# Optimization experiments

Measured on AMD Instinct MI355X. Metric: run time of the kernel, lower is better.

Reference implementation:

```python
import jax, jax.numpy as jnp
import numpy as np

N = 100000   # nodes
E = 1600000  # edges (avg degree 16)
G = 512      # graphs in batch
IN = 96      # in_channels
H = 128      # hidden_channels
C = 100      # num_classes
ED = 8       # edge_dim
L = 4        # num_layers
EPS_LN = 1e-5


def setup_inputs() -> dict:
    key = jax.random.key(0)
    ks = jax.random.split(key, 24)
    s = 0.05
    d = {
        "x": jax.random.normal(ks[0], (N, IN), jnp.float32),
        "edge_index": jax.random.randint(ks[1], (2, E), 0, N, jnp.int32),
        "batch": jnp.sort(jax.random.randint(ks[2], (N,), 0, G, jnp.int32)),
        "edge_attr": jax.random.normal(ks[3], (E, ED), jnp.float32),
        # edge encoder MLP: Linear(ED,H) -> ReLU -> Linear(H,1)
        "ee_W1": jax.random.normal(ks[4], (ED, H), jnp.float32) * s,
        "ee_b1": jnp.zeros((H,), jnp.float32),
        "ee_W2": jax.random.normal(ks[5], (H, 1), jnp.float32) * s,
        "ee_b2": jnp.zeros((1,), jnp.float32),
        # GCNConv weights (PyG: lin without bias, bias added after aggregation)
        "W0": jax.random.normal(ks[6], (IN, H), jnp.float32) * s,
        "cb0": jnp.zeros((H,), jnp.float32),
        "W1": jax.random.normal(ks[7], (H, H), jnp.float32) * s,
        "cb1": jnp.zeros((H,), jnp.float32),
        "W2": jax.random.normal(ks[8], (H, H), jnp.float32) * s,
        "cb2": jnp.zeros((H,), jnp.float32),
        "W3": jax.random.normal(ks[9], (H, H), jnp.float32) * s,
        "cb3": jnp.zeros((H,), jnp.float32),
        # LayerNorm params
        "g0": jnp.ones((H,), jnp.float32), "be0": jnp.zeros((H,), jnp.float32),
        "g1": jnp.ones((H,), jnp.float32), "be1": jnp.zeros((H,), jnp.float32),
        "g2": jnp.ones((H,), jnp.float32), "be2": jnp.zeros((H,), jnp.float32),
        "g3": jnp.ones((H,), jnp.float32), "be3": jnp.zeros((H,), jnp.float32),
        # residual projection for layer 0 only (IN != H)
        "res_W": jax.random.normal(ks[10], (IN, H), jnp.float32) * s,
        "res_b": jnp.zeros((H,), jnp.float32),
        # head: Linear(2H,H) -> ReLU -> Linear(H,C)
        "hW1": jax.random.normal(ks[11], (2 * H, H), jnp.float32) * s,
        "hb1": jnp.zeros((H,), jnp.float32),
        "hW2": jax.random.normal(ks[12], (H, C), jnp.float32) * s,
        "hb2": jnp.zeros((C,), jnp.float32),
    }
    return d


def _layer_norm(h, g, b):
    mu = jnp.mean(h, axis=-1, keepdims=True)
    var = jnp.mean(jnp.square(h - mu), axis=-1, keepdims=True)
    return g * (h - mu) / jnp.sqrt(var + EPS_LN) + b


def reference(x, edge_index, batch, edge_attr,
              ee_W1, ee_b1, ee_W2, ee_b2,
              W0, cb0, W1, cb1, W2, cb2, W3, cb3,
              g0, be0, g1, be1, g2, be2, g3, be3,
              res_W, res_b, hW1, hb1, hW2, hb2):
    row, col = edge_index[0], edge_index[1]

    # edge weight = softplus(MLP(edge_attr)) + 1e-4  -> [E]
    eh = jax.nn.relu(edge_attr @ ee_W1 + ee_b1)
    ew = jax.nn.softplus((eh @ ee_W2 + ee_b2)[:, 0]) + 1e-4

    # add self loops with weight 1 (PyG GCNConv default)
    loops = jnp.arange(N, dtype=row.dtype)
    row_sl = jnp.concatenate([row, loops])
    col_sl = jnp.concatenate([col, loops])
    ew_sl = jnp.concatenate([ew, jnp.ones((N,), ew.dtype)])

    # symmetric normalization: D^-1/2 A D^-1/2 (deg over target index)
    deg = jax.ops.segment_sum(ew_sl, col_sl, num_segments=N)
    dis = jnp.where(deg > 0, jax.lax.rsqrt(deg), 0.0)
    norm = dis[row_sl] * ew_sl * dis[col_sl]  # [E+N]

    def conv(h, W, b):
        hw = h @ W                                   # [N,H]
        msg = hw[row_sl] * norm[:, None]             # [E+N,H]
        return jax.ops.segment_sum(msg, col_sl, num_segments=N) + b

    Ws = [W0, W1, W2, W3]
    cbs = [cb0, cb1, cb2, cb3]
    gs = [g0, g1, g2, g3]
    bes = [be0, be1, be2, be3]

    hidden = []
    cur = x
    for i in range(L):
        h = conv(cur, Ws[i], cbs[i])
        h = _layer_norm(h, gs[i], bes[i])
        res = cur @ res_W + res_b if i == 0 else cur
        h = jax.nn.relu(h + res)
        # dropout: eval mode -> identity
        hidden.append(h)
        cur = h
    xm = jnp.mean(jnp.stack(hidden, axis=0), axis=0)  # [N,H]

    # meanmax pooling over graphs
    counts = jax.ops.segment_sum(jnp.ones((N,), xm.dtype), batch, num_segments=G)
    gmean = jax.ops.segment_sum(xm, batch, num_segments=G) / jnp.maximum(counts, 1.0)[:, None]
    gmax = jax.ops.segment_max(xm, batch, num_segments=G)
    gmax = jnp.where(jnp.isfinite(gmax), gmax, 0.0)
    g = jnp.concatenate([gmean, gmax], axis=-1)       # [G,2H]

    # head (dropout identity in eval)
    return jax.nn.relu(g @ hW1 + hb1) @ hW2 + hb2     # [G,C]
```

## Files before the change

### kernel.cpp

```cpp
#include <hip/hip_runtime.h>
#include <hip/hip_fp16.h>
#include <math.h>

#define NN 100000
#define EE 1600000
#define GB 512
#define INC 96
#define HH 128
#define CC 100
#define MAXD 64
#define BUCKB 9
#define NBUK 196
#define CAPB 10240
#define EB 4096

typedef __bf16 bf16x8 __attribute__((ext_vector_type(8)));
typedef _Float16 f16x8 __attribute__((ext_vector_type(8)));
typedef float f32x4 __attribute__((ext_vector_type(4)));

__device__ __forceinline__ float unpack_w_f32(unsigned v) {
    return __half2float(__ushort_as_half((unsigned short)(v & 0x7FFFu)));
}
__device__ __forceinline__ __half2 unpack_w_h2(unsigned v) {
    __half h = __ushort_as_half((unsigned short)(v & 0x7FFFu));
    return __halves2half2(h, h);
}

__global__ __launch_bounds__(256) void k_cast(const float* __restrict__ src, __half* __restrict__ dst, int n4) {
    int i = blockIdx.x * 256 + threadIdx.x;
    if (i >= n4) return;
    float4 v = *(const float4*)&src[(size_t)i * 4];
    __half2 a = __floats2half2_rn(v.x, v.y);
    __half2 b = __floats2half2_rn(v.z, v.w);
    *(__half2*)&dst[(size_t)i * 4]     = a;
    *(__half2*)&dst[(size_t)i * 4 + 2] = b;
}

__global__ __launch_bounds__(256) void k_prep_weights(
    const float* __restrict__ W0, const float* __restrict__ resW,
    const float* __restrict__ W1m, const float* __restrict__ W2m, const float* __restrict__ W3m,
    __half* __restrict__ wt0, __half* __restrict__ wtR,
    __half* __restrict__ wt1, __half* __restrict__ wt2, __half* __restrict__ wt3)
{
    int idx = blockIdx.x * 256 + threadIdx.x;
    const float* src; __half* dst; int K, base;
    if (idx < 12288)      { src = W0;   dst = wt0; K = 96;  base = 0; }
    else if (idx < 24576) { src = resW; dst = wtR; K = 96;  base = 12288; }
    else if (idx < 40960) { src = W1m;  dst = wt1; K = 128; base = 24576; }
    else if (idx < 57344) { src = W2m;  dst = wt2; K = 128; base = 40960; }
    else if (idx < 73728) { src = W3m;  dst = wt3; K = 128; base = 57344; }
    else return;
    int l = idx - base;
    int k = l >> 7, n = l & 127;
    dst[(size_t)n * K + k] = __float2half(src[l]);
}

__global__ __launch_bounds__(512) void k_prep_w1(const float* __restrict__ W1, __bf16* __restrict__ w1f) {
    int tid = threadIdx.x;
    int t = tid >> 6, lane = tid & 63;
    int ln15 = lane & 15, quad = lane >> 4;
    bf16x8 v = {};
    if (quad == 0) {
#pragma unroll
        for (int j = 0; j < 8; ++j) v[j] = (__bf16)W1[j * 128 + t * 16 + ln15];
    }
    *(bf16x8*)&w1f[(size_t)(t * 64 + lane) * 8] = v;
}

__global__ __launch_bounds__(256) void k_edge_mlp_mfma(
    const float* __restrict__ ea,
    const __bf16* __restrict__ w1f, const float* __restrict__ b1,
    const float* __restrict__ W2, const float* __restrict__ b2,
    __half* __restrict__ ew)
{
    __shared__ float sDot[128];
    int tid = threadIdx.x, wva = tid >> 6, lane = tid & 63;
    int ln15 = lane & 15, quad = lane >> 4;
    int ebase = blockIdx.x * 128 + wva * 32;

    bf16x8 bfr[8];
#pragma unroll
    for (int t = 0; t < 8; ++t) bfr[t] = *(const bf16x8*)&w1f[(size_t)(t * 64 + lane) * 8];

    bf16x8 a0 = {}, a1 = {};
    if (quad == 0) {
        const float* p0 = &ea[(size_t)(ebase + ln15) * 8];
        float4 u0 = *(const float4*)p0, u1 = *(const float4*)(p0 + 4);
        a0[0] = (__bf16)u0.x; a0[1] = (__bf16)u0.y; a0[2] = (__bf16)u0.z; a0[3] = (__bf16)u0.w;
        a0[4] = (__bf16)u1.x; a0[5] = (__bf16)u1.y; a0[6] = (__bf16)u1.z; a0[7] = (__bf16)u1.w;
        const float* p1 = &ea[(size_t)(ebase + 16 + ln15) * 8];
        float4 w0 = *(const float4*)p1, w1v = *(const float4*)(p1 + 4);
        a1[0] = (__bf16)w0.x; a1[1] = (__bf16)w0.y; a1[2] = (__bf16)w0.z; a1[3] = (__bf16)w0.w;
        a1[4] = (__bf16)w1v.x; a1[5] = (__bf16)w1v.y; a1[6] = (__bf16)w1v.z; a1[7] = (__bf16)w1v.w;
    }

    f32x4 d0 = {0.f, 0.f, 0.f, 0.f}, d1 = {0.f, 0.f, 0.f, 0.f};
#pragma unroll
    for (int t = 0; t < 8; ++t) {
        f32x4 z = {0.f, 0.f, 0.f, 0.f};
        f32x4 c0 = __builtin_amdgcn_mfma_f32_16x16x32_bf16(a0, bfr[t], z, 0, 0, 0);
        f32x4 c1 = __builtin_amdgcn_mfma_f32_16x16x32_bf16(a1, bfr[t], z, 0, 0, 0);
        int col = t * 16 + ln15;
        float b1v = b1[col], w2v = W2[col];
#pragma unroll
        for (int r = 0; r < 4; ++r) {
            float v0 = fmaxf(c0[r] + b1v, 0.0f);
            float v1 = fmaxf(c1[r] + b1v, 0.0f);
            d0[r] = fmaf(v0, w2v, d0[r]);
            d1[r] = fmaf(v1, w2v, d1[r]);
        }
    }
#pragma unroll
    for (int o = 1; o < 16; o <<= 1) {
#pragma unroll
        for (int r = 0; r < 4; ++r) {
            d0[r] += __shfl_xor(d0[r], o, 64);
            d1[r] += __shfl_xor(d1[r], o, 64);
        }
    }
    if (ln15 == 0) {
#pragma unroll
        for (int r = 0; r < 4; ++r) {
            sDot[wva * 32 + quad * 4 + r]      = d0[r];
            sDot[wva * 32 + 16 + quad * 4 + r] = d1[r];
        }
    }
    __syncthreads();
    if (tid < 128) {
        int e = blockIdx.x * 128 + tid;
        float x = sDot[tid] + b2[0];
        float sp = (x > 20.0f) ? x : log1pf(expf(x));
        ew[e] = __float2half(sp + 1e-4f);
    }
}

__global__ __launch_bounds__(256) void k_split(const int* __restrict__ ei, const __half* __restrict__ ew,
                                               int* __restrict__ cntB, uint2* __restrict__ barr) {
    __shared__ unsigned hist[NBUK];
    __shared__ unsigned gbase[NBUK];
    __shared__ unsigned short rloc[EB];
    int tid = threadIdx.x;
    for (int b = tid; b < NBUK; b += 256) hist[b] = 0;
    __syncthreads();
    int e0 = blockIdx.x * EB;
#pragma unroll
    for (int j = 0; j < EB / 256; ++j) {
        int e = e0 + j * 256 + tid;
        if (e < EE) {
            int c = ei[EE + e];
            rloc[j * 256 + tid] = (unsigned short)atomicAdd(&hist[c >> BUCKB], 1u);
        }
    }
    __syncthreads();
    for (int b = tid; b < NBUK; b += 256)
        gbase[b] = (hist[b] > 0) ? (unsigned)atomicAdd(&cntB[b], (int)hist[b]) : 0u;
    __syncthreads();
#pragma unroll
    for (int j = 0; j < EB / 256; ++j) {
        int e = e0 + j * 256 + tid;
        if (e < EE) {
            int c = ei[EE + e];
            int b = c >> BUCKB;
            unsigned pos = gbase[b] + rloc[j * 256 + tid];
            if (pos < CAPB) {
                unsigned hb = (unsigned)__half_as_ushort(ew[e]) & 0x7FFFu;
                barr[(size_t)b * CAPB + pos] = make_uint2(((unsigned)c << 15) | hb, (unsigned)ei[e]);
            }
        }
    }
}

__global__ __launch_bounds__(256) void k_build(const int* __restrict__ cntB, const uint2* __restrict__ barr,
                                               unsigned* __restrict__ epack, int* __restrict__ cnt,
                                               float* __restrict__ dis) {
    __shared__ unsigned ncnt[512];
    __shared__ float ndeg[512];
    int tid = threadIdx.x, b = blockIdx.x;
    for (int i = tid; i < 512; i += 256) { ncnt[i] = 0; ndeg[i] = 0.0f; }
    __syncthreads();
    int n0 = b << BUCKB;
    int m = cntB[b]; if (m > CAPB) m = CAPB;
    for (int i = tid; i < m; i += 256) {
        uint2 rec = barr[(size_t)b * CAPB + i];
        int c = (int)(rec.x >> 15);
        int cl = c - n0;
        unsigned rank = atomicAdd(&ncnt[cl], 1u);
        if (rank < MAXD) epack[(size_t)c * MAXD + rank] = (rec.y << 15) | (rec.x & 0x7FFFu);
        atomicAdd(&ndeg[cl], unpack_w_f32(rec.x));
    }
    __syncthreads();
    int nn = NN - n0; if (nn > 512) nn = 512;
    for (int i = tid; i < nn; i += 256) {
        unsigned cc = ncnt[i]; if (cc > MAXD) cc = MAXD;
        cnt[n0 + i] = (int)cc;
        dis[n0 + i] = rsqrtf(1.0f + ndeg[i]);
    }
}

__global__ __launch_bounds__(256) void k_norm(const int* __restrict__ cnt, const float* __restrict__ dis,
                                              unsigned* __restrict__ epack, int n) {
    int wv = threadIdx.x >> 6, lane = threadIdx.x & 63;
    int i = blockIdx.x * 4 + wv;
    if (i >= n) return;
    float dc = dis[i];
    if (lane < cnt[i]) {
        unsigned v = epack[(size_t)i * MAXD + lane];
        float wn = dis[v >> 15] * unpack_w_f32(v) * dc;
        unsigned hb = (unsigned)__half_as_ushort(__float2half(wn)) & 0x7FFFu;
        epack[(size_t)i * MAXD + lane] = (v & 0xFFFF8000u) | hb;
    }
}

__global__ __launch_bounds__(256) void k_gemm_f16(
    const __half* __restrict__ A, const __half* __restrict__ Bt,
    const float* __restrict__ bias, __half* __restrict__ C, int M, int K)
{
    int tid = threadIdx.x;
    int wv = tid >> 6, lane = tid & 63;
    int ln15 = lane & 15, quad = lane >> 4;
    int m0 = blockIdx.x * 64;
    int n0 = wv * 32;
    f32x4 acc[4][2];
#pragma unroll
    for (int mt = 0; mt < 4; ++mt)
#pragma unroll
        for (int nt = 0; nt < 2; ++nt) acc[mt][nt] = (f32x4){0.f, 0.f, 0.f, 0.f};

    int rowm[4];
#pragma unroll
    for (int mt = 0; mt < 4; ++mt) {
        int r = m0 + mt * 16 + ln15;
        rowm[mt] = r < M ? r : M - 1;
    }
    for (int kc = 0; kc < K; kc += 32) {
        f16x8 af[4], bfr[2];
#pragma unroll
        for (int mt = 0; mt < 4; ++mt)
            af[mt] = *(const f16x8*)&A[(size_t)rowm[mt] * K + kc + quad * 8];
#pragma unroll
        for (int nt = 0; nt < 2; ++nt)
            bfr[nt] = *(const f16x8*)&Bt[(size_t)(n0 + nt * 16 + ln15) * K + kc + quad * 8];
#pragma unroll
        for (int mt = 0; mt < 4; ++mt)
#pragma unroll
            for (int nt = 0; nt < 2; ++nt)
                acc[mt][nt] = __builtin_amdgcn_mfma_f32_16x16x32_f16(af[mt], bfr[nt], acc[mt][nt], 0, 0, 0);
    }
#pragma unroll
    for (int nt = 0; nt < 2; ++nt) {
        int col = n0 + nt * 16 + ln15;
        float bv = bias ? bias[col] : 0.0f;
#pragma unroll
        for (int mt = 0; mt < 4; ++mt) {
#pragma unroll
            for (int r = 0; r < 4; ++r) {
                int row = m0 + mt * 16 + quad * 4 + r;
                if (row < M) C[(size_t)row * 128 + col] = __float2half(acc[mt][nt][r] + bv);
            }
        }
    }
}

__global__ __launch_bounds__(256) void k_agg_ln(
    const __half* __restrict__ hw, const float* __restrict__ dis,
    const int* __restrict__ cnt, const unsigned* __restrict__ epack,
    const float* __restrict__ cb, const float* __restrict__ gam,
    const float* __restrict__ bet, const __half* __restrict__ res,
    __half* __restrict__ out, int n)
{
    int wv = threadIdx.x >> 6;
    int lane = threadIdx.x & 63;
    int i = blockIdx.x * 4 + wv;
    if (i >= n) return;
    float di = dis[i];
    float sn = di * di;
    __half2 own = *(const __half2*)&hw[(size_t)i * HH + lane * 2];
    __half hsn = __float2half(sn);
    __half2 acc = __hmul2(own, __halves2half2(hsn, hsn));
    int cn = cnt[i];
    const unsigned* ebase = &epack[(size_t)i * MAXD];
    int k = 0;
    for (; k + 8 <= cn; k += 8) {
        uint4 q0 = *(const uint4*)&ebase[k];
        uint4 q1 = *(const uint4*)&ebase[k + 4];
        __half2 v0 = *(const __half2*)&hw[(size_t)(q0.x >> 15) * HH + lane * 2];
        __half2 v1 = *(const __half2*)&hw[(size_t)(q0.y >> 15) * HH + lane * 2];
        __half2 v2 = *(const __half2*)&hw[(size_t)(q0.z >> 15) * HH + lane * 2];
        __half2 v3 = *(const __half2*)&hw[(size_t)(q0.w >> 15) * HH + lane * 2];
        __half2 v4 = *(const __half2*)&hw[(size_t)(q1.x >> 15) * HH + lane * 2];
        __half2 v5 = *(const __half2*)&hw[(size_t)(q1.y >> 15) * HH + lane * 2];
        __half2 v6 = *(const __half2*)&hw[(size_t)(q1.z >> 15) * HH + lane * 2];
        __half2 v7 = *(const __half2*)&hw[(size_t)(q1.w >> 15) * HH + lane * 2];
        acc = __hfma2(v0, unpack_w_h2(q0.x), acc);
        acc = __hfma2(v1, unpack_w_h2(q0.y), acc);
        acc = __hfma2(v2, unpack_w_h2(q0.z), acc);
        acc = __hfma2(v3, unpack_w_h2(q0.w), acc);
        acc = __hfma2(v4, unpack_w_h2(q1.x), acc);
        acc = __hfma2(v5, unpack_w_h2(q1.y), acc);
        acc = __hfma2(v6, unpack_w_h2(q1.z), acc);
        acc = __hfma2(v7, unpack_w_h2(q1.w), acc);
    }
    for (; k < cn; ++k) {
        unsigned e = ebase[k];
        __half2 v = *(const __half2*)&hw[(size_t)(e >> 15) * HH + lane * 2];
        acc = __hfma2(v, unpack_w_h2(e), acc);
    }
    float2 af = __half22float2(acc);
    float2 cbv = *(const float2*)&cb[lane * 2];
    af.x += cbv.x; af.y += cbv.y;
    float s1 = af.x + af.y;
    float s2 = af.x * af.x + af.y * af.y;
#pragma unroll
    for (int o = 32; o > 0; o >>= 1) {
        s1 += __shfl_xor(s1, o, 64);
        s2 += __shfl_xor(s2, o, 64);
    }
    float mean = s1 * (1.0f / HH);
    float var = fmaxf(s2 * (1.0f / HH) - mean * mean, 0.0f);
    float rstd = rsqrtf(var + 1e-5f);
    float2 gv = *(const float2*)&gam[lane * 2];
    float2 bv = *(const float2*)&bet[lane * 2];
    float2 rv = __half22float2(*(const __half2*)&res[(size_t)i * HH + lane * 2]);
    float hx = fmaxf(fmaf(gv.x, (af.x - mean) * rstd, bv.x) + rv.x, 0.0f);
    float hy = fmaxf(fmaf(gv.y, (af.y - mean) * rstd, bv.y) + rv.y, 0.0f);
    *(__half2*)&out[(size_t)i * HH + lane * 2] = __floats2half2_rn(hx, hy);
}

__global__ __launch_bounds__(512) void k_pool(
    const __half* __restrict__ l0, const __half* __restrict__ l1,
    const __half* __restrict__ l2, const __half* __restrict__ l3,
    const int* __restrict__ batch, float* __restrict__ gbuf, int n)
{
    __shared__ float ssum[8][128];
    __shared__ float smax[8][128];
    int g = blockIdx.x, tid = threadIdx.x;
    int grp = tid >> 6, lane = tid & 63;
    int lo = 0, hi = n;
    while (lo < hi) { int m = (lo + hi) >> 1; if (batch[m] < g) lo = m + 1; else hi = m; }
    int start = lo;
    lo = start; hi = n;
    while (lo < hi) { int m = (lo + hi) >> 1; if (batch[m] < g + 1) lo = m + 1; else hi = m; }
    int end = lo;
    float sx = 0.0f, sy = 0.0f, mx = -INFINITY, my = -INFINITY;
    for (int nd = start + grp; nd < end; nd += 8) {
        size_t off = (size_t)nd * HH + lane * 2;
        float2 v0 = __half22float2(*(const __half2*)&l0[off]);
        float2 v1 = __half22float2(*(const __half2*)&l1[off]);
        float2 v2 = __half22float2(*(const __half2*)&l2[off]);
        float2 v3 = __half22float2(*(const __half2*)&l3[off]);
        float vx = (v0.x + v1.x + v2.x + v3.x) * 0.25f;
        float vy = (v0.y + v1.y + v2.y + v3.y) * 0.25f;
        sx += vx; sy += vy;
        mx = fmaxf(mx, vx); my = fmaxf(my, vy);
    }
    ssum[grp][lane * 2] = sx; ssum[grp][lane * 2 + 1] = sy;
    smax[grp][lane * 2] = mx; smax[grp][lane * 2 + 1] = my;
    __syncthreads();
    if (tid < 128) {
        float s = 0.0f, m = -INFINITY;
#pragma unroll
        for (int j = 0; j < 8; ++j) {
            s += ssum[j][tid];
            m = fmaxf(m, smax[j][tid]);
        }
        int cntg = end - start;
        gbuf[(size_t)g * 256 + tid] = s / fmaxf((float)cntg, 1.0f);
        gbuf[(size_t)g * 256 + 128 + tid] = (cntg > 0) ? m : 0.0f;
    }
}

__global__ __launch_bounds__(128) void k_head(const float* __restrict__ gbuf,
                                              const float* __restrict__ hW1, const float* __restrict__ hb1,
                                              const float* __restrict__ hW2, const float* __restrict__ hb2,
                                              float* __restrict__ out) {
    __shared__ __align__(16) float sg[256];
    __shared__ __align__(16) float sh[128];
    int g = blockIdx.x, t = threadIdx.x;
    sg[t] = gbuf[(size_t)g * 256 + t];
    sg[t + 128] = gbuf[(size_t)g * 256 + 128 + t];
    __syncthreads();
    float h = hb1[t];
    for (int k = 0; k < 256; ++k) h = fmaf(sg[k], hW1[(size_t)k * 128 + t], h);
    sh[t] = fmaxf(h, 0.0f);
    __syncthreads();
    if (t < 100) {
        float o = hb2[t];
        for (int k = 0; k < 128; ++k) o = fmaf(sh[k], hW2[(size_t)k * 100 + t], o);
        out[(size_t)g * 100 + t] = o;
    }
}

extern "C" void kernel_launch(void* const* d_in, const int* in_sizes, int n_in,
                              void* d_out, int out_size, void* d_ws, size_t ws_size,
                              hipStream_t stream) {
    const float* x     = (const float*)d_in[0];
    const int*   ei    = (const int*)d_in[1];
    const int*   batch = (const int*)d_in[2];
    const float* ea    = (const float*)d_in[3];
    const float* eeW1  = (const float*)d_in[4];
    const float* eeb1  = (const float*)d_in[5];
    const float* eeW2  = (const float*)d_in[6];
    const float* eeb2  = (const float*)d_in[7];
    const float* W[4]  = {(const float*)d_in[8], (const float*)d_in[10], (const float*)d_in[12], (const float*)d_in[14]};
    const float* cb[4] = {(const float*)d_in[9], (const float*)d_in[11], (const float*)d_in[13], (const float*)d_in[15]};
    const float* gm[4] = {(const float*)d_in[16], (const float*)d_in[18], (const float*)d_in[20], (const float*)d_in[22]};
    const float* be[4] = {(const float*)d_in[17], (const float*)d_in[19], (const float*)d_in[21], (const float*)d_in[23]};
    const float* resW  = (const float*)d_in[24];
    const float* resb  = (const float*)d_in[25];
    const float* hW1   = (const float*)d_in[26];
    const float* hb1   = (const float*)d_in[27];
    const float* hW2   = (const float*)d_in[28];
    const float* hb2   = (const float*)d_in[29];
    float* out = (float*)d_out;

    char* w = (char*)d_ws;
    auto alloc = [&](size_t bytes) { void* p = w; w += (bytes + 255) & ~(size_t)255; return p; };
    __half*   ew     = (__half*)  alloc((size_t)EE * 2);
    float*    dis    = (float*)   alloc((size_t)NN * 4);
    int*      cnt    = (int*)     alloc((size_t)NN * 4);
    int*      cntB   = (int*)     alloc((size_t)NBUK * 4);
    uint2*    barr   = (uint2*)   alloc((size_t)NBUK * CAPB * 8);
    unsigned* epack  = (unsigned*)alloc((size_t)NN * MAXD * 4);
    __half*   xb     = (__half*)  alloc((size_t)NN * INC * 2);
    __half*   hw     = (__half*)  alloc((size_t)NN * HH * 2);
    __half*   lout[4];
    for (int i = 0; i < 4; ++i) lout[i] = (__half*)alloc((size_t)NN * HH * 2);
    float*    gbuf   = (float*)   alloc((size_t)GB * 256 * 4);
    __half*   wt0    = (__half*)  alloc((size_t)INC * HH * 2);
    __half*   wtR    = (__half*)  alloc((size_t)INC * HH * 2);
    __half*   wt1    = (__half*)  alloc((size_t)HH * HH * 2);
    __half*   wt2    = (__half*)  alloc((size_t)HH * HH * 2);
    __half*   wt3    = (__half*)  alloc((size_t)HH * HH * 2);
    __bf16*   w1f    = (__bf16*)  alloc((size_t)8 * 64 * 8 * 2);
    __half*   wtc[4] = {wt0, wt1, wt2, wt3};
    __half*   res0   = lout[1];

    int nblkEdge = EE / 128;
    int nblkSplit = (EE + EB - 1) / EB;
    int nblkGemm = (NN + 63) / 64;
    int nblkCast = (NN * INC / 4 + 255) / 256;

    hipMemsetAsync(cntB, 0, (size_t)NBUK * 4, stream);
    k_cast<<<nblkCast, 256, 0, stream>>>(x, xb, NN * INC / 4);
    k_prep_weights<<<288, 256, 0, stream>>>(W[0], resW, W[1], W[2], W[3], wt0, wtR, wt1, wt2, wt3);
    k_prep_w1<<<1, 512, 0, stream>>>(eeW1, w1f);
    k_edge_mlp_mfma<<<nblkEdge, 256, 0, stream>>>(ea, w1f, eeb1, eeW2, eeb2, ew);
    k_split<<<nblkSplit, 256, 0, stream>>>(ei, ew, cntB, barr);
    k_build<<<NBUK, 256, 0, stream>>>(cntB, barr, epack, cnt, dis);
    k_norm<<<(NN + 3) / 4, 256, 0, stream>>>(cnt, dis, epack, NN);

    k_gemm_f16<<<nblkGemm, 256, 0, stream>>>(xb, wt0, nullptr, hw, NN, INC);
    k_gemm_f16<<<nblkGemm, 256, 0, stream>>>(xb, wtR, resb, res0, NN, INC);
    k_agg_ln<<<(NN + 3) / 4, 256, 0, stream>>>(hw, dis, cnt, epack,
                                               cb[0], gm[0], be[0], res0, lout[0], NN);
    for (int l = 1; l < 4; ++l) {
        k_gemm_f16<<<nblkGemm, 256, 0, stream>>>(lout[l - 1], wtc[l], nullptr, hw, NN, HH);
        k_agg_ln<<<(NN + 3) / 4, 256, 0, stream>>>(hw, dis, cnt, epack,
                                                   cb[l], gm[l], be[l], lout[l - 1], lout[l], NN);
    }

    k_pool<<<GB, 512, 0, stream>>>(lout[0], lout[1], lout[2], lout[3], batch, gbuf, NN);
    k_head<<<GB, 128, 0, stream>>>(gbuf, hW1, hb1, hW2, hb2, out);
}
```

Before: 774.2 us.

## Split agg wave into half-waves over edges; fuse prep and pool+head kernels

The aggregation kernel now has each half-wave process alternate edges, with each lane loading 8 bytes (4 features) per neighbour row. The two halves are combined with a cross-half shuffle before LayerNorm. The aim is to issue fewer, wider gather loads per edge and overlap two neighbour fetches per instruction. Separately, the two weight-prep kernels are merged into one and the head MLP is fused into the pooling kernel, which removes two launches and the gbuf round trip. Padding slots past the count fall back to a self record whose weight is zero, and the epack buffer grows slightly to cover the reads.

```diff
diff --git a/kernel.cpp b/kernel.cpp
--- a/kernel.cpp
+++ b/kernel.cpp
@@ -25,6 +25,12 @@
     __half h = __ushort_as_half((unsigned short)(v & 0x7FFFu));
     return __halves2half2(h, h);
 }
+__device__ __forceinline__ void load_h2x2(const __half* p, __half2& a, __half2& b) {
+    uint2 u = *(const uint2*)p;
+    union { unsigned u; __half2 h; } ua, ub;
+    ua.u = u.x; ub.u = u.y;
+    a = ua.h; b = ub.h;
+}
 
 __global__ __launch_bounds__(256) void k_cast(const float* __restrict__ src, __half* __restrict__ dst, int n4) {
     int i = blockIdx.x * 256 + threadIdx.x;
@@ -36,13 +42,28 @@
     *(__half2*)&dst[(size_t)i * 4 + 2] = b;
 }
 
-__global__ __launch_bounds__(256) void k_prep_weights(
+__global__ __launch_bounds__(512) void k_prep(
     const float* __restrict__ W0, const float* __restrict__ resW,
     const float* __restrict__ W1m, const float* __restrict__ W2m, const float* __restrict__ W3m,
+    const float* __restrict__ eeW1,
     __half* __restrict__ wt0, __half* __restrict__ wtR,
-    __half* __restrict__ wt1, __half* __restrict__ wt2, __half* __restrict__ wt3)
+    __half* __restrict__ wt1, __half* __restrict__ wt2, __half* __restrict__ wt3,
+    __bf16* __restrict__ w1f)
 {
-    int idx = blockIdx.x * 256 + threadIdx.x;
+    int tid = threadIdx.x;
+    if (blockIdx.x == 288) {
+        int t = tid >> 6, lane = tid & 63;
+        int ln15 = lane & 15, quad = lane >> 4;
+        bf16x8 v = {};
+        if (quad == 0) {
+#pragma unroll
+            for (int j = 0; j < 8; ++j) v[j] = (__bf16)eeW1[j * 128 + t * 16 + ln15];
+        }
+        *(bf16x8*)&w1f[(size_t)(t * 64 + lane) * 8] = v;
+        return;
+    }
+    if (tid >= 256) return;
+    int idx = blockIdx.x * 256 + tid;
     const float* src; __half* dst; int K, base;
     if (idx < 12288)      { src = W0;   dst = wt0; K = 96;  base = 0; }
     else if (idx < 24576) { src = resW; dst = wtR; K = 96;  base = 12288; }
@@ -53,18 +74,6 @@
     int l = idx - base;
     int k = l >> 7, n = l & 127;
     dst[(size_t)n * K + k] = __float2half(src[l]);
-}
-
-__global__ __launch_bounds__(512) void k_prep_w1(const float* __restrict__ W1, __bf16* __restrict__ w1f) {
-    int tid = threadIdx.x;
-    int t = tid >> 6, lane = tid & 63;
-    int ln15 = lane & 15, quad = lane >> 4;
-    bf16x8 v = {};
-    if (quad == 0) {
-#pragma unroll
-        for (int j = 0; j < 8; ++j) v[j] = (__bf16)W1[j * 128 + t * 16 + ln15];
-    }
-    *(bf16x8*)&w1f[(size_t)(t * 64 + lane) * 8] = v;
 }
 
 __global__ __launch_bounds__(256) void k_edge_mlp_mfma(
@@ -272,67 +281,84 @@
     int lane = threadIdx.x & 63;
     int i = blockIdx.x * 4 + wv;
     if (i >= n) return;
+    int hf = lane >> 5;
+    int l32 = lane & 31;
+    size_t foff = (size_t)(l32 << 2);
+
     float di = dis[i];
     float sn = di * di;
-    __half2 own = *(const __half2*)&hw[(size_t)i * HH + lane * 2];
-    __half hsn = __float2half(sn);
-    __half2 acc = __hmul2(own, __halves2half2(hsn, hsn));
+
+    __half2 acc0, acc1;
+    {
+        __half2 v0, v1;
+        load_h2x2(&hw[(size_t)i * HH + foff], v0, v1);
+        __half ws = __float2half(hf ? 0.0f : sn);
+        __half2 wh = __halves2half2(ws, ws);
+        acc0 = __hmul2(v0, wh);
+        acc1 = __hmul2(v1, wh);
+    }
     int cn = cnt[i];
     const unsigned* ebase = &epack[(size_t)i * MAXD];
-    int k = 0;
-    for (; k + 8 <= cn; k += 8) {
-        uint4 q0 = *(const uint4*)&ebase[k];
-        uint4 q1 = *(const uint4*)&ebase[k + 4];
-        __half2 v0 = *(const __half2*)&hw[(size_t)(q0.x >> 15) * HH + lane * 2];
-        __half2 v1 = *(const __half2*)&hw[(size_t)(q0.y >> 15) * HH + lane * 2];
-        __half2 v2 = *(const __half2*)&hw[(size_t)(q0.z >> 15) * HH + lane * 2];
-        __half2 v3 = *(const __half2*)&hw[(size_t)(q0.w >> 15) * HH + lane * 2];
-        __half2 v4 = *(const __half2*)&hw[(size_t)(q1.x >> 15) * HH + lane * 2];
-        __half2 v5 = *(const __half2*)&hw[(size_t)(q1.y >> 15) * HH + lane * 2];
-        __half2 v6 = *(const __half2*)&hw[(size_t)(q1.z >> 15) * HH + lane * 2];
-        __half2 v7 = *(const __half2*)&hw[(size_t)(q1.w >> 15) * HH + lane * 2];
-        acc = __hfma2(v0, unpack_w_h2(q0.x), acc);
-        acc = __hfma2(v1, unpack_w_h2(q0.y), acc);
-        acc = __hfma2(v2, unpack_w_h2(q0.z), acc);
-        acc = __hfma2(v3, unpack_w_h2(q0.w), acc);
-        acc = __hfma2(v4, unpack_w_h2(q1.x), acc);
-        acc = __hfma2(v5, unpack_w_h2(q1.y), acc);
-        acc = __hfma2(v6, unpack_w_h2(q1.z), acc);
-        acc = __hfma2(v7, unpack_w_h2(q1.w), acc);
-    }
-    for (; k < cn; ++k) {
-        unsigned e = ebase[k];
-        __half2 v = *(const __half2*)&hw[(size_t)(e >> 15) * HH + lane * 2];
-        acc = __hfma2(v, unpack_w_h2(e), acc);
-    }
-    float2 af = __half22float2(acc);
-    float2 cbv = *(const float2*)&cb[lane * 2];
-    af.x += cbv.x; af.y += cbv.y;
-    float s1 = af.x + af.y;
-    float s2 = af.x * af.x + af.y * af.y;
-#pragma unroll
-    for (int o = 32; o > 0; o >>= 1) {
+    unsigned selfrec = (unsigned)i << 15;
+    for (int k = 0; k < cn; k += 16) {
+#pragma unroll
+        for (int p = 0; p < 8; ++p) {
+            int idx = k + (p << 1) + hf;
+            unsigned rec = (idx < cn) ? ebase[idx] : selfrec;
+            __half2 v0, v1;
+            load_h2x2(&hw[(size_t)(rec >> 15) * HH + foff], v0, v1);
+            __half2 wh = unpack_w_h2(rec);
+            acc0 = __hfma2(v0, wh, acc0);
+            acc1 = __hfma2(v1, wh, acc1);
+        }
+    }
+    float2 f0 = __half22float2(acc0);
+    float2 f1 = __half22float2(acc1);
+    f0.x += __shfl_xor(f0.x, 32, 64);
+    f0.y += __shfl_xor(f0.y, 32, 64);
+    f1.x += __shfl_xor(f1.x, 32, 64);
+    f1.y += __shfl_xor(f1.y, 32, 64);
+    float4 cbv = *(const float4*)&cb[foff];
+    f0.x += cbv.x; f0.y += cbv.y; f1.x += cbv.z; f1.y += cbv.w;
+    float s1 = f0.x + f0.y + f1.x + f1.y;
+    float s2 = f0.x * f0.x + f0.y * f0.y + f1.x * f1.x + f1.y * f1.y;
+#pragma unroll
+    for (int o = 1; o < 32; o <<= 1) {
         s1 += __shfl_xor(s1, o, 64);
         s2 += __shfl_xor(s2, o, 64);
     }
     float mean = s1 * (1.0f / HH);
     float var = fmaxf(s2 * (1.0f / HH) - mean * mean, 0.0f);
     float rstd = rsqrtf(var + 1e-5f);
-    float2 gv = *(const float2*)&gam[lane * 2];
-    float2 bv = *(const float2*)&bet[lane * 2];
-    float2 rv = __half22float2(*(const __half2*)&res[(size_t)i * HH + lane * 2]);
-    float hx = fmaxf(fmaf(gv.x, (af.x - mean) * rstd, bv.x) + rv.x, 0.0f);
-    float hy = fmaxf(fmaf(gv.y, (af.y - mean) * rstd, bv.y) + rv.y, 0.0f);
-    *(__half2*)&out[(size_t)i * HH + lane * 2] = __floats2half2_rn(hx, hy);
-}
-
-__global__ __launch_bounds__(512) void k_pool(
+    float4 gv = *(const float4*)&gam[foff];
+    float4 bv = *(const float4*)&bet[foff];
+    __half2 r0, r1;
+    load_h2x2(&res[(size_t)i * HH + foff], r0, r1);
+    float2 rf0 = __half22float2(r0), rf1 = __half22float2(r1);
+    float o0 = fmaxf(fmaf(gv.x, (f0.x - mean) * rstd, bv.x) + rf0.x, 0.0f);
+    float o1 = fmaxf(fmaf(gv.y, (f0.y - mean) * rstd, bv.y) + rf0.y, 0.0f);
+    float o2 = fmaxf(fmaf(gv.z, (f1.x - mean) * rstd, bv.z) + rf1.x, 0.0f);
+    float o3 = fmaxf(fmaf(gv.w, (f1.y - mean) * rstd, bv.w) + rf1.y, 0.0f);
+    if (hf == 0) {
+        union { __half2 h[2]; uint2 u; } pk;
+        pk.h[0] = __floats2half2_rn(o0, o1);
+        pk.h[1] = __floats2half2_rn(o2, o3);
+        *(uint2*)&out[(size_t)i * HH + foff] = pk.u;
+    }
+}
+
+__global__ __launch_bounds__(512) void k_pool_head(
     const __half* __restrict__ l0, const __half* __restrict__ l1,
     const __half* __restrict__ l2, const __half* __restrict__ l3,
-    const int* __restrict__ batch, float* __restrict__ gbuf, int n)
+    const int* __restrict__ batch,
+    const float* __restrict__ hW1, const float* __restrict__ hb1,
+    const float* __restrict__ hW2, const float* __restrict__ hb2,
+    float* __restrict__ out, int n)
 {
     __shared__ float ssum[8][128];
     __shared__ float smax[8][128];
+    __shared__ __align__(16) float sg[256];
+    __shared__ __align__(16) float sh[128];
     int g = blockIdx.x, tid = threadIdx.x;
     int grp = tid >> 6, lane = tid & 63;
     int lo = 0, hi = n;
@@ -364,29 +390,20 @@
             m = fmaxf(m, smax[j][tid]);
         }
         int cntg = end - start;
-        gbuf[(size_t)g * 256 + tid] = s / fmaxf((float)cntg, 1.0f);
-        gbuf[(size_t)g * 256 + 128 + tid] = (cntg > 0) ? m : 0.0f;
-    }
-}
-
-__global__ __launch_bounds__(128) void k_head(const float* __restrict__ gbuf,
-                                              const float* __restrict__ hW1, const float* __restrict__ hb1,
-                                              const float* __restrict__ hW2, const float* __restrict__ hb2,
-                                              float* __restrict__ out) {
-    __shared__ __align__(16) float sg[256];
-    __shared__ __align__(16) float sh[128];
-    int g = blockIdx.x, t = threadIdx.x;
-    sg[t] = gbuf[(size_t)g * 256 + t];
-    sg[t + 128] = gbuf[(size_t)g * 256 + 128 + t];
-    __syncthreads();
-    float h = hb1[t];
-    for (int k = 0; k < 256; ++k) h = fmaf(sg[k], hW1[(size_t)k * 128 + t], h);
-    sh[t] = fmaxf(h, 0.0f);
-    __syncthreads();
-    if (t < 100) {
-        float o = hb2[t];
-        for (int k = 0; k < 128; ++k) o = fmaf(sh[k], hW2[(size_t)k * 100 + t], o);
-        out[(size_t)g * 100 + t] = o;
+        sg[tid] = s / fmaxf((float)cntg, 1.0f);
+        sg[128 + tid] = (cntg > 0) ? m : 0.0f;
+    }
+    __syncthreads();
+    if (tid < 128) {
+        float h = hb1[tid];
+        for (int k = 0; k < 256; ++k) h = fmaf(sg[k], hW1[(size_t)k * 128 + tid], h);
+        sh[tid] = fmaxf(h, 0.0f);
+    }
+    __syncthreads();
+    if (tid < 100) {
+        float o = hb2[tid];
+        for (int k = 0; k < 128; ++k) o = fmaf(sh[k], hW2[(size_t)k * 100 + tid], o);
+        out[(size_t)g * 100 + tid] = o;
     }
 }
 
@@ -420,12 +437,11 @@
     int*      cnt    = (int*)     alloc((size_t)NN * 4);
     int*      cntB   = (int*)     alloc((size_t)NBUK * 4);
     uint2*    barr   = (uint2*)   alloc((size_t)NBUK * CAPB * 8);
-    unsigned* epack  = (unsigned*)alloc((size_t)NN * MAXD * 4);
+    unsigned* epack  = (unsigned*)alloc((size_t)(NN * MAXD + 64) * 4);
     __half*   xb     = (__half*)  alloc((size_t)NN * INC * 2);
     __half*   hw     = (__half*)  alloc((size_t)NN * HH * 2);
     __half*   lout[4];
     for (int i = 0; i < 4; ++i) lout[i] = (__half*)alloc((size_t)NN * HH * 2);
-    float*    gbuf   = (float*)   alloc((size_t)GB * 256 * 4);
     __half*   wt0    = (__half*)  alloc((size_t)INC * HH * 2);
     __half*   wtR    = (__half*)  alloc((size_t)INC * HH * 2);
     __half*   wt1    = (__half*)  alloc((size_t)HH * HH * 2);
@@ -442,8 +458,8 @@
 
     hipMemsetAsync(cntB, 0, (size_t)NBUK * 4, stream);
     k_cast<<<nblkCast, 256, 0, stream>>>(x, xb, NN * INC / 4);
-    k_prep_weights<<<288, 256, 0, stream>>>(W[0], resW, W[1], W[2], W[3], wt0, wtR, wt1, wt2, wt3);
-    k_prep_w1<<<1, 512, 0, stream>>>(eeW1, w1f);
+    k_prep<<<289, 512, 0, stream>>>(W[0], resW, W[1], W[2], W[3], eeW1,
+                                    wt0, wtR, wt1, wt2, wt3, w1f);
     k_edge_mlp_mfma<<<nblkEdge, 256, 0, stream>>>(ea, w1f, eeb1, eeW2, eeb2, ew);
     k_split<<<nblkSplit, 256, 0, stream>>>(ei, ew, cntB, barr);
     k_build<<<NBUK, 256, 0, stream>>>(cntB, barr, epack, cnt, dis);
@@ -459,6 +475,6 @@
                                                    cb[l], gm[l], be[l], lout[l - 1], lout[l], NN);
     }
 
-    k_pool<<<GB, 512, 0, stream>>>(lout[0], lout[1], lout[2], lout[3], batch, gbuf, NN);
-    k_head<<<GB, 128, 0, stream>>>(gbuf, hW1, hb1, hW2, hb2, out);
-}
+    k_pool_head<<<GB, 512, 0, stream>>>(lout[0], lout[1], lout[2], lout[3], batch,
+                                        hW1, hb1, hW2, hb2, out, NN);
+}
```

Result: slower. 830.6 us (+7.3%).
